# Optimization experiments

Hardware: AMD Instinct MI355X
Metric: run time of the kernel (lower is better)

The kernel has to match this reference:

```python
import jax, jax.numpy as jnp
import numpy as np

N_NODES = 100000
N_EDGES = 1600000
IN_CH = 256
OUT_CH = 32
HEADS = 4
NEG_SLOPE = 0.2


def setup_inputs() -> dict:
    key = jax.random.key(0)
    k1, k2, k3, k4, k5 = jax.random.split(key, 5)
    x = jax.random.normal(k1, (N_NODES, IN_CH), dtype=jnp.float32)
    edge_index = jax.random.randint(k2, (2, N_EDGES), 0, N_NODES, dtype=jnp.int64)
    hc = HEADS * OUT_CH
    # glorot init like the torch module
    std_w = np.sqrt(6.0 / (hc + IN_CH))
    W = jax.random.uniform(k3, (hc, IN_CH), dtype=jnp.float32, minval=-std_w, maxval=std_w)
    b = jnp.zeros((hc,), dtype=jnp.float32)
    std_a = np.sqrt(6.0 / (hc + 2))
    att = jax.random.uniform(k4, (hc, 2), dtype=jnp.float32, minval=-std_a, maxval=std_a)
    return {"x": x, "edge_index": edge_index, "W": W, "b": b, "att": att}


def reference(x, edge_index, W, b, att):
    # flow = 'target_to_source': tid=0, sid=1
    tar = edge_index[0]
    src = edge_index[1]
    feat = x @ W.T + b                      # [N, H*C]
    e_pre = feat @ att                      # [N, 2]
    e_src = e_pre[:, 0:1]                   # [N, 1]
    e_tar = e_pre[:, 1:2]                   # [N, 1]
    # edge scores
    e = jnp.exp(jax.nn.leaky_relu(e_src[src] + e_tar[tar], negative_slope=NEG_SLOPE))   # [E, 1]
    e_self = jnp.exp(jax.nn.leaky_relu(e_src + e_tar, negative_slope=NEG_SLOPE))        # [N, 1]
    # softmax denominator over incoming edges + self loop
    e_sum = jax.ops.segment_sum(e, tar, num_segments=N_NODES) + e_self                  # [N, 1]
    alpha_self = e_self / e_sum             # [N, 1]
    alpha = e / e_sum[tar]                  # [E, 1]
    # weighted aggregation (dropout=0 / eval -> identity)
    out = jax.ops.segment_sum(feat[src] * alpha, tar, num_segments=N_NODES)
    out = out + feat * alpha_self           # [N, H*C], concat=True
    return out
```

## Files before the change

kernel.cpp:

```cpp
#include <hip/hip_runtime.h>
#include <hip/hip_bf16.h>
#include <math.h>

#define N_NODES 100000
#define N_EDGES 1600000
#define IN_CH 256
#define HC 128
#define NEG_SLOPE 0.2f

#define NB_C 196
#define CCAP 8704
#define CHUNK 6400

typedef __attribute__((ext_vector_type(8))) short short8;
typedef __attribute__((ext_vector_type(4))) float floatx4;

__device__ inline ushort f2b(float f) {
    __hip_bfloat16 h = __float2bfloat16(f);
    return *(ushort*)&h;
}

#define GBM 128

__global__ __launch_bounds__(256, 2)
void gemm_mfma(const float* __restrict__ x, const float* __restrict__ W,
               const float* __restrict__ b, const float* __restrict__ att,
               __hip_bfloat16* __restrict__ featb,
               float* __restrict__ e_src, float* __restrict__ e_tar,
               float* __restrict__ e_self) {
    __shared__ ushort xs[128][72];
    __shared__ ushort wsh[128][72];

    const int tid  = threadIdx.x;
    const int wave = tid >> 6;
    const int lane = tid & 63;
    const int l16  = lane >> 4;
    const int lc   = lane & 15;
    const int row0 = blockIdx.x * GBM;

    floatx4 acc[2][8];
    #pragma unroll
    for (int mt = 0; mt < 2; ++mt)
        #pragma unroll
        for (int nt = 0; nt < 8; ++nt)
            acc[mt][nt] = (floatx4){0.f, 0.f, 0.f, 0.f};

    for (int kb = 0; kb < 4; ++kb) {
        const int r  = tid >> 4;
        const int kq = tid & 15;
        #pragma unroll
        for (int i = 0; i < 8; ++i) {
            int rr = r + i * 16;
            int gr = row0 + rr;
            float4 v = make_float4(0.f, 0.f, 0.f, 0.f);
            if (gr < N_NODES)
                v = *(const float4*)&x[(size_t)gr * IN_CH + kb * 64 + kq * 4];
            ushort4 u;
            u.x = f2b(v.x); u.y = f2b(v.y); u.z = f2b(v.z); u.w = f2b(v.w);
            *(ushort4*)&xs[rr][kq * 4] = u;
        }
        #pragma unroll
        for (int i = 0; i < 8; ++i) {
            int rr = r + i * 16;
            float4 v = *(const float4*)&W[(size_t)rr * IN_CH + kb * 64 + kq * 4];
            ushort4 u;
            u.x = f2b(v.x); u.y = f2b(v.y); u.z = f2b(v.z); u.w = f2b(v.w);
            *(ushort4*)&wsh[rr][kq * 4] = u;
        }
        __syncthreads();
        #pragma unroll
        for (int ks = 0; ks < 2; ++ks) {
            short8 a0 = *(short8*)&xs[wave * 32 + lc][ks * 32 + l16 * 8];
            short8 a1 = *(short8*)&xs[wave * 32 + 16 + lc][ks * 32 + l16 * 8];
            short8 bf[8];
            #pragma unroll
            for (int nt = 0; nt < 8; ++nt)
                bf[nt] = *(short8*)&wsh[nt * 16 + lc][ks * 32 + l16 * 8];
            #pragma unroll
            for (int nt = 0; nt < 8; ++nt) {
                acc[0][nt] = __builtin_amdgcn_mfma_f32_16x16x32_bf16(a0, bf[nt], acc[0][nt], 0, 0, 0);
                acc[1][nt] = __builtin_amdgcn_mfma_f32_16x16x32_bf16(a1, bf[nt], acc[1][nt], 0, 0, 0);
            }
        }
        __syncthreads();
    }

    float av0[8], av1[8], bc[8];
    #pragma unroll
    for (int nt = 0; nt < 8; ++nt) {
        float2 av = *(const float2*)&att[(nt * 16 + lc) * 2];
        av0[nt] = av.x; av1[nt] = av.y;
        bc[nt] = b[nt * 16 + lc];
    }

    #pragma unroll
    for (int mt = 0; mt < 2; ++mt) {
        #pragma unroll
        for (int rg = 0; rg < 4; ++rg) {
            int row = row0 + wave * 32 + mt * 16 + l16 * 4 + rg;
            float s = 0.f, t = 0.f;
            float vals[8];
            #pragma unroll
            for (int nt = 0; nt < 8; ++nt) {
                float v = acc[mt][nt][rg] + bc[nt];
                vals[nt] = v;
                s += v * av0[nt];
                t += v * av1[nt];
            }
            #pragma unroll
            for (int off = 8; off; off >>= 1) {
                s += __shfl_xor(s, off);
                t += __shfl_xor(t, off);
            }
            if (row < N_NODES) {
                if (lc == 0) {
                    e_src[row] = s;
                    e_tar[row] = t;
                    float z = s + t;
                    float lr = z > 0.f ? z : NEG_SLOPE * z;
                    e_self[row] = __expf(lr);
                }
                #pragma unroll
                for (int nt = 0; nt < 8; ++nt)
                    featb[(size_t)row * HC + nt * 16 + lc] = __float2bfloat16(vals[nt]);
            }
        }
    }
}

__global__ __launch_bounds__(256)
void bin2_k(const int* __restrict__ ei, int* __restrict__ gcur,
            int* __restrict__ ebuf) {
    __shared__ int lcnt[NB_C];
    __shared__ int lcur[NB_C];
    const int base = blockIdx.x * CHUNK;

    for (int i = threadIdx.x; i < NB_C; i += 256) lcnt[i] = 0;
    __syncthreads();

    for (int i = threadIdx.x; i < CHUNK; i += 256)
        atomicAdd(&lcnt[ei[base + i] >> 9], 1);
    __syncthreads();

    for (int bkt = threadIdx.x; bkt < NB_C; bkt += 256) {
        int c = lcnt[bkt];
        lcur[bkt] = c ? atomicAdd(&gcur[bkt], c) : 0;
    }
    __syncthreads();

    for (int i = threadIdx.x; i < CHUNK; i += 256) {
        int t = ei[base + i];
        int s = ei[N_EDGES + base + i];
        int bkt = t >> 9;
        int pos = atomicAdd(&lcur[bkt], 1);
        if (pos < CCAP)
            ebuf[bkt * CCAP + pos] = s | ((t & 511) << 17);
    }
}

__global__ void cscan_k(const int* __restrict__ gcur, int* __restrict__ nbase) {
    if (threadIdx.x == 0 && blockIdx.x == 0) {
        int run = 0;
        for (int i = 0; i < NB_C; ++i) {
            nbase[i] = run;
            int c = gcur[i]; if (c > CCAP) c = CCAP;
            run += c;
        }
        nbase[NB_C] = run;
    }
}

__global__ __launch_bounds__(256)
void bucket_csr2_k(const int* __restrict__ gcur, const int* __restrict__ nbase,
                   const int* __restrict__ ebuf, int* __restrict__ offsets,
                   int* __restrict__ csr_src) {
    const int b = blockIdx.x;
    int count = gcur[b]; if (count > CCAP) count = CCAP;
    const int base = nbase[b];
    const int tid = threadIdx.x;

    __shared__ int lcnt[512];
    __shared__ int lofs[512];
    __shared__ int lout[CCAP];

    lcnt[tid] = 0; lcnt[tid + 256] = 0;
    __syncthreads();

    const int* st = &ebuf[b * CCAP];
    for (int i = tid; i < count; i += 256)
        atomicAdd(&lcnt[st[i] >> 17], 1);
    __syncthreads();

    lofs[tid] = lcnt[tid]; lofs[tid + 256] = lcnt[tid + 256];
    __syncthreads();
    for (int off = 1; off < 512; off <<= 1) {
        int i0 = tid, i1 = tid + 256;
        int a0 = lofs[i0] + ((i0 >= off) ? lofs[i0 - off] : 0);
        int a1 = lofs[i1] + lofs[i1 - off];
        __syncthreads();
        lofs[i0] = a0; lofs[i1] = a1;
        __syncthreads();
    }
    int e0 = lofs[tid] - lcnt[tid];
    int e1 = lofs[tid + 256] - lcnt[tid + 256];
    __syncthreads();
    lcnt[tid] = e0; lcnt[tid + 256] = e1;

    int node0 = b * 512;
    {
        int n0 = node0 + tid, n1 = node0 + tid + 256;
        if (n0 < N_NODES) offsets[n0] = base + e0;
        if (n1 < N_NODES) offsets[n1] = base + e1;
    }
    if (b == NB_C - 1 && tid == 0) offsets[N_NODES] = base + count;
    __syncthreads();

    for (int i = tid; i < count; i += 256) {
        int v = st[i];
        int pos = atomicAdd(&lcnt[v >> 17], 1);
        lout[pos] = v & 0x1FFFF;
    }
    __syncthreads();

    for (int i = tid; i < count; i += 256)
        csr_src[base + i] = lout[i];
}

__device__ inline float edge_e(float z) {
    float lr = z > 0.f ? z : NEG_SLOPE * z;
    return __expf(lr);
}

__global__ __launch_bounds__(256)
void aggregate_k(const int* __restrict__ offsets, const int* __restrict__ csr_src,
                 const float* __restrict__ e_src, const float* __restrict__ e_tar,
                 const __hip_bfloat162* __restrict__ featb,
                 const float* __restrict__ e_self, float* __restrict__ out) {
    int node = blockIdx.x * 4 + (threadIdx.x >> 6);
    if (node >= N_NODES) return;
    int lane = threadIdx.x & 63;
    int beg = offsets[node];
    int end = offsets[node + 1];
    float et = e_tar[node];
    float eself = e_self[node];

    float2 fs = __bfloat1622float2(featb[(size_t)node * 64 + lane]);
    float esum = eself;
    float accx = eself * fs.x, accy = eself * fs.y;

    int j = beg;
    for (; j + 3 < end; j += 4) {
        int s0 = csr_src[j];
        int s1 = csr_src[j + 1];
        int s2 = csr_src[j + 2];
        int s3 = csr_src[j + 3];
        float e0 = edge_e(e_src[s0] + et);
        float e1 = edge_e(e_src[s1] + et);
        float e2 = edge_e(e_src[s2] + et);
        float e3 = edge_e(e_src[s3] + et);
        float2 f0 = __bfloat1622float2(featb[(size_t)s0 * 64 + lane]);
        float2 f1 = __bfloat1622float2(featb[(size_t)s1 * 64 + lane]);
        float2 f2 = __bfloat1622float2(featb[(size_t)s2 * 64 + lane]);
        float2 f3 = __bfloat1622float2(featb[(size_t)s3 * 64 + lane]);
        esum += (e0 + e1) + (e2 + e3);
        accx += e0 * f0.x + e1 * f1.x + e2 * f2.x + e3 * f3.x;
        accy += e0 * f0.y + e1 * f1.y + e2 * f2.y + e3 * f3.y;
    }
    for (; j < end; ++j) {
        int s0 = csr_src[j];
        float e0 = edge_e(e_src[s0] + et);
        float2 f0 = __bfloat1622float2(featb[(size_t)s0 * 64 + lane]);
        esum += e0;
        accx += e0 * f0.x;
        accy += e0 * f0.y;
    }
    float inv = 1.f / esum;
    *(float2*)&out[(size_t)node * HC + lane * 2] = make_float2(accx * inv, accy * inv);
}

extern "C" void kernel_launch(void* const* d_in, const int* in_sizes, int n_in,
                              void* d_out, int out_size, void* d_ws, size_t ws_size,
                              hipStream_t stream) {
    const float* x   = (const float*)d_in[0];
    const int*   ei  = (const int*)d_in[1];
    const float* W   = (const float*)d_in[2];
    const float* b   = (const float*)d_in[3];
    const float* att = (const float*)d_in[4];
    float* out = (float*)d_out;

    __hip_bfloat16* featb = (__hip_bfloat16*)d_ws;
    float* e_src   = (float*)(featb + (size_t)N_NODES * HC);
    float* e_tar   = e_src   + N_NODES;
    float* e_self  = e_tar   + N_NODES;
    int*   offsets = (int*)(e_self + N_NODES);
    int*   gcur    = offsets + N_NODES + 1;
    int*   nbase   = gcur    + NB_C;
    int*   csr_src = nbase   + NB_C + 1;
    int*   ebuf    = csr_src + N_EDGES;

    (void)hipMemsetAsync(gcur, 0, NB_C * sizeof(int), stream);

    bin2_k<<<N_EDGES / CHUNK, 256, 0, stream>>>(ei, gcur, ebuf);
    cscan_k<<<1, 64, 0, stream>>>(gcur, nbase);
    bucket_csr2_k<<<NB_C, 256, 0, stream>>>(gcur, nbase, ebuf, offsets, csr_src);

    gemm_mfma<<<(N_NODES + GBM - 1) / GBM, 256, 0, stream>>>(x, W, b, att, featb,
                                                             e_src, e_tar, e_self);

    aggregate_k<<<(N_NODES + 3) / 4, 256, 0, stream>>>(offsets, csr_src, e_src, e_tar,
                                                       (const __hip_bfloat162*)featb,
                                                       e_self, out);
}
```

Measured before the change: 322.8 us.

## Fuse bucket scan into CSR kernel, widen blocks, vectorize aggregate index loads

After: 303.5 us. -6.0%, faster.

```diff
diff --git a/kernel.cpp b/kernel.cpp
--- a/kernel.cpp
+++ b/kernel.cpp
@@ -10,7 +10,7 @@
 
 #define NB_C 196
 #define CCAP 8704
-#define CHUNK 6400
+#define CHUNK 3200
 
 typedef __attribute__((ext_vector_type(8))) short short8;
 typedef __attribute__((ext_vector_type(4))) float floatx4;
@@ -158,71 +158,66 @@
     }
 }
 
-__global__ void cscan_k(const int* __restrict__ gcur, int* __restrict__ nbase) {
-    if (threadIdx.x == 0 && blockIdx.x == 0) {
-        int run = 0;
-        for (int i = 0; i < NB_C; ++i) {
-            nbase[i] = run;
-            int c = gcur[i]; if (c > CCAP) c = CCAP;
-            run += c;
-        }
-        nbase[NB_C] = run;
-    }
-}
-
-__global__ __launch_bounds__(256)
-void bucket_csr2_k(const int* __restrict__ gcur, const int* __restrict__ nbase,
-                   const int* __restrict__ ebuf, int* __restrict__ offsets,
-                   int* __restrict__ csr_src) {
+__global__ __launch_bounds__(512)
+void bucket_csr2_k(const int* __restrict__ gcur, const int* __restrict__ ebuf,
+                   int* __restrict__ offsets, int* __restrict__ csr_src) {
     const int b = blockIdx.x;
-    int count = gcur[b]; if (count > CCAP) count = CCAP;
-    const int base = nbase[b];
     const int tid = threadIdx.x;
 
+    __shared__ int sc[256];
     __shared__ int lcnt[512];
     __shared__ int lofs[512];
     __shared__ int lout[CCAP];
 
-    lcnt[tid] = 0; lcnt[tid + 256] = 0;
-    __syncthreads();
+    if (tid < 256) {
+        int c = 0;
+        if (tid < NB_C) { c = gcur[tid]; if (c > CCAP) c = CCAP; }
+        sc[tid] = c;
+    }
+    lcnt[tid] = 0;
+    __syncthreads();
+    #pragma unroll
+    for (int off = 1; off < 256; off <<= 1) {
+        int v = 0;
+        if (tid < 256) v = sc[tid] + ((tid >= off) ? sc[tid - off] : 0);
+        __syncthreads();
+        if (tid < 256) sc[tid] = v;
+        __syncthreads();
+    }
+    int count = gcur[b]; if (count > CCAP) count = CCAP;
+    const int base = (b == 0) ? 0 : sc[b - 1];
 
     const int* st = &ebuf[b * CCAP];
-    for (int i = tid; i < count; i += 256)
+    for (int i = tid; i < count; i += 512)
         atomicAdd(&lcnt[st[i] >> 17], 1);
     __syncthreads();
 
-    lofs[tid] = lcnt[tid]; lofs[tid + 256] = lcnt[tid + 256];
+    lofs[tid] = lcnt[tid];
     __syncthreads();
     for (int off = 1; off < 512; off <<= 1) {
-        int i0 = tid, i1 = tid + 256;
-        int a0 = lofs[i0] + ((i0 >= off) ? lofs[i0 - off] : 0);
-        int a1 = lofs[i1] + lofs[i1 - off];
-        __syncthreads();
-        lofs[i0] = a0; lofs[i1] = a1;
-        __syncthreads();
-    }
-    int e0 = lofs[tid] - lcnt[tid];
-    int e1 = lofs[tid + 256] - lcnt[tid + 256];
-    __syncthreads();
-    lcnt[tid] = e0; lcnt[tid + 256] = e1;
-
-    int node0 = b * 512;
+        int v = lofs[tid] + ((tid >= off) ? lofs[tid - off] : 0);
+        __syncthreads();
+        lofs[tid] = v;
+        __syncthreads();
+    }
+    int excl = lofs[tid] - lcnt[tid];
+    lcnt[tid] = excl;
+
     {
-        int n0 = node0 + tid, n1 = node0 + tid + 256;
-        if (n0 < N_NODES) offsets[n0] = base + e0;
-        if (n1 < N_NODES) offsets[n1] = base + e1;
+        int n0 = b * 512 + tid;
+        if (n0 < N_NODES) offsets[n0] = base + excl;
     }
     if (b == NB_C - 1 && tid == 0) offsets[N_NODES] = base + count;
     __syncthreads();
 
-    for (int i = tid; i < count; i += 256) {
+    for (int i = tid; i < count; i += 512) {
         int v = st[i];
         int pos = atomicAdd(&lcnt[v >> 17], 1);
         lout[pos] = v & 0x1FFFF;
     }
     __syncthreads();
 
-    for (int i = tid; i < count; i += 256)
+    for (int i = tid; i < count; i += 512)
         csr_src[base + i] = lout[i];
 }
 
@@ -249,19 +244,47 @@
     float accx = eself * fs.x, accy = eself * fs.y;
 
     int j = beg;
+    int npeel = (4 - (j & 3)) & 3;
+    if (npeel > end - j) npeel = end - j;
+    for (int p = 0; p < npeel; ++p, ++j) {
+        int s0 = csr_src[j];
+        float e0 = edge_e(e_src[s0] + et);
+        float2 f0 = __bfloat1622float2(featb[(size_t)s0 * 64 + lane]);
+        esum += e0; accx += e0 * f0.x; accy += e0 * f0.y;
+    }
+
+    for (; j + 7 < end; j += 8) {
+        int4 a = *(const int4*)&csr_src[j];
+        int4 c = *(const int4*)&csr_src[j + 4];
+        float p0 = e_src[a.x], p1 = e_src[a.y], p2 = e_src[a.z], p3 = e_src[a.w];
+        float p4 = e_src[c.x], p5 = e_src[c.y], p6 = e_src[c.z], p7 = e_src[c.w];
+        float2 f0 = __bfloat1622float2(featb[(size_t)a.x * 64 + lane]);
+        float2 f1 = __bfloat1622float2(featb[(size_t)a.y * 64 + lane]);
+        float2 f2 = __bfloat1622float2(featb[(size_t)a.z * 64 + lane]);
+        float2 f3 = __bfloat1622float2(featb[(size_t)a.w * 64 + lane]);
+        float2 f4 = __bfloat1622float2(featb[(size_t)c.x * 64 + lane]);
+        float2 f5 = __bfloat1622float2(featb[(size_t)c.y * 64 + lane]);
+        float2 f6 = __bfloat1622float2(featb[(size_t)c.z * 64 + lane]);
+        float2 f7 = __bfloat1622float2(featb[(size_t)c.w * 64 + lane]);
+        float e0 = edge_e(p0 + et), e1 = edge_e(p1 + et);
+        float e2 = edge_e(p2 + et), e3 = edge_e(p3 + et);
+        float e4 = edge_e(p4 + et), e5 = edge_e(p5 + et);
+        float e6 = edge_e(p6 + et), e7 = edge_e(p7 + et);
+        esum += ((e0 + e1) + (e2 + e3)) + ((e4 + e5) + (e6 + e7));
+        accx += e0 * f0.x + e1 * f1.x + e2 * f2.x + e3 * f3.x;
+        accx += e4 * f4.x + e5 * f5.x + e6 * f6.x + e7 * f7.x;
+        accy += e0 * f0.y + e1 * f1.y + e2 * f2.y + e3 * f3.y;
+        accy += e4 * f4.y + e5 * f5.y + e6 * f6.y + e7 * f7.y;
+    }
     for (; j + 3 < end; j += 4) {
-        int s0 = csr_src[j];
-        int s1 = csr_src[j + 1];
-        int s2 = csr_src[j + 2];
-        int s3 = csr_src[j + 3];
-        float e0 = edge_e(e_src[s0] + et);
-        float e1 = edge_e(e_src[s1] + et);
-        float e2 = edge_e(e_src[s2] + et);
-        float e3 = edge_e(e_src[s3] + et);
-        float2 f0 = __bfloat1622float2(featb[(size_t)s0 * 64 + lane]);
-        float2 f1 = __bfloat1622float2(featb[(size_t)s1 * 64 + lane]);
-        float2 f2 = __bfloat1622float2(featb[(size_t)s2 * 64 + lane]);
-        float2 f3 = __bfloat1622float2(featb[(size_t)s3 * 64 + lane]);
+        int4 a = *(const int4*)&csr_src[j];
+        float p0 = e_src[a.x], p1 = e_src[a.y], p2 = e_src[a.z], p3 = e_src[a.w];
+        float2 f0 = __bfloat1622float2(featb[(size_t)a.x * 64 + lane]);
+        float2 f1 = __bfloat1622float2(featb[(size_t)a.y * 64 + lane]);
+        float2 f2 = __bfloat1622float2(featb[(size_t)a.z * 64 + lane]);
+        float2 f3 = __bfloat1622float2(featb[(size_t)a.w * 64 + lane]);
+        float e0 = edge_e(p0 + et), e1 = edge_e(p1 + et);
+        float e2 = edge_e(p2 + et), e3 = edge_e(p3 + et);
         esum += (e0 + e1) + (e2 + e3);
         accx += e0 * f0.x + e1 * f1.x + e2 * f2.x + e3 * f3.x;
         accy += e0 * f0.y + e1 * f1.y + e2 * f2.y + e3 * f3.y;
@@ -288,21 +311,25 @@
     const float* att = (const float*)d_in[4];
     float* out = (float*)d_out;
 
-    __hip_bfloat16* featb = (__hip_bfloat16*)d_ws;
-    float* e_src   = (float*)(featb + (size_t)N_NODES * HC);
-    float* e_tar   = e_src   + N_NODES;
-    float* e_self  = e_tar   + N_NODES;
-    int*   offsets = (int*)(e_self + N_NODES);
-    int*   gcur    = offsets + N_NODES + 1;
-    int*   nbase   = gcur    + NB_C;
-    int*   csr_src = nbase   + NB_C + 1;
-    int*   ebuf    = csr_src + N_EDGES;
+    unsigned char* p = (unsigned char*)d_ws;
+    auto take = [&](size_t bytes) {
+        unsigned char* r = p;
+        p += (bytes + 255) & ~(size_t)255;
+        return (void*)r;
+    };
+    __hip_bfloat16* featb = (__hip_bfloat16*)take((size_t)N_NODES * HC * sizeof(__hip_bfloat16));
+    float* e_src   = (float*)take((size_t)N_NODES * sizeof(float));
+    float* e_tar   = (float*)take((size_t)N_NODES * sizeof(float));
+    float* e_self  = (float*)take((size_t)N_NODES * sizeof(float));
+    int*   offsets = (int*)take((size_t)(N_NODES + 1) * sizeof(int));
+    int*   gcur    = (int*)take((size_t)NB_C * sizeof(int));
+    int*   csr_src = (int*)take((size_t)N_EDGES * sizeof(int));
+    int*   ebuf    = (int*)take((size_t)NB_C * CCAP * sizeof(int));
 
     (void)hipMemsetAsync(gcur, 0, NB_C * sizeof(int), stream);
 
     bin2_k<<<N_EDGES / CHUNK, 256, 0, stream>>>(ei, gcur, ebuf);
-    cscan_k<<<1, 64, 0, stream>>>(gcur, nbase);
-    bucket_csr2_k<<<NB_C, 256, 0, stream>>>(gcur, nbase, ebuf, offsets, csr_src);
+    bucket_csr2_k<<<NB_C, 512, 0, stream>>>(gcur, ebuf, offsets, csr_src);
 
     gemm_mfma<<<(N_NODES + GBM - 1) / GBM, 256, 0, stream>>>(x, W, b, att, featb,
                                                              e_src, e_tar, e_self);
```
